# Kernel optimization log

Measured on AMD Instinct MI355X. Metric: run time of the kernel, lower is better.

Reference implementation:

```python
import jax, jax.numpy as jnp
import numpy as np

N_NODES = 4096
N_EDGES = 8192
N_GRAPHS = 256
D_NODE = 64
D_EDGE = 32
H = 256


def setup_inputs() -> dict:
    key = jax.random.key(0)
    ks = jax.random.split(key, 16)
    s = lambda d: 1.0 / np.sqrt(d)
    inp = {
        "x": jax.random.normal(ks[0], (N_NODES, D_NODE), dtype=jnp.float32),
        "edge_index": jax.random.randint(ks[1], (2, N_EDGES), 0, N_NODES),
        "edge_attr": jax.random.normal(ks[2], (N_EDGES, D_EDGE), dtype=jnp.float32),
        "batch": jnp.sort(jax.random.randint(ks[3], (N_NODES,), 0, N_GRAPHS)),
        # conv1: edge MLP 32 -> 64*256, root weight 64->256, bias 256
        "nn1_w": jax.random.normal(ks[4], (D_EDGE, D_NODE * H), dtype=jnp.float32) * s(D_EDGE),
        "nn1_b": jnp.zeros((D_NODE * H,), dtype=jnp.float32),
        "root1_w": jax.random.normal(ks[5], (D_NODE, H), dtype=jnp.float32) * s(D_NODE),
        "bias1": jnp.zeros((H,), dtype=jnp.float32),
        # conv2: edge MLP 32 -> 256*256, root weight 256->256, bias 256
        "nn2_w": jax.random.normal(ks[6], (D_EDGE, H * H), dtype=jnp.float32) * s(D_EDGE),
        "nn2_b": jnp.zeros((H * H,), dtype=jnp.float32),
        "root2_w": jax.random.normal(ks[7], (H, H), dtype=jnp.float32) * s(H),
        "bias2": jnp.zeros((H,), dtype=jnp.float32),
        # readout MLP: 256 -> 128 -> 1
        "lin1_w": jax.random.normal(ks[8], (H, H // 2), dtype=jnp.float32) * s(H),
        "lin1_b": jnp.zeros((H // 2,), dtype=jnp.float32),
        "lin2_w": jax.random.normal(ks[9], (H // 2, 1), dtype=jnp.float32) * s(H // 2),
        "lin2_b": jnp.zeros((1,), dtype=jnp.float32),
    }
    return inp


def nnconv(x, src, dst, edge_attr, nn_w, nn_b, root_w, bias, out_c):
    # PyG NNConv (aggr='add'): per-edge weight matrix from edge MLP,
    # message = x[src] @ W_e, scatter-add at dst, plus root transform + bias.
    e = edge_attr.shape[0]
    in_c = x.shape[1]
    w_e = (edge_attr @ nn_w + nn_b).reshape(e, in_c, out_c)  # [E, in, out]
    msg = jnp.einsum('ei,eio->eo', x[src], w_e)              # [E, out]
    agg = jax.ops.segment_sum(msg, dst, num_segments=x.shape[0])
    return agg + x @ root_w + bias


def reference(x, edge_index, edge_attr, batch,
              nn1_w, nn1_b, root1_w, bias1,
              nn2_w, nn2_b, root2_w, bias2,
              lin1_w, lin1_b, lin2_w, lin2_b):
    src, dst = edge_index[0], edge_index[1]
    h = nnconv(x, src, dst, edge_attr, nn1_w, nn1_b, root1_w, bias1, H)
    h = jax.nn.relu(h)
    h = nnconv(h, src, dst, edge_attr, nn2_w, nn2_b, root2_w, bias2, H)
    # global mean pool over graphs
    sums = jax.ops.segment_sum(h, batch, num_segments=N_GRAPHS)
    cnts = jax.ops.segment_sum(jnp.ones((h.shape[0],), h.dtype), batch, num_segments=N_GRAPHS)
    pooled = sums / jnp.maximum(cnts, 1.0)[:, None]
    # dropout is identity in eval mode
    z = jax.nn.relu(pooled @ lin1_w + lin1_b)
    return jax.nn.sigmoid(z @ lin2_w + lin2_b)  # [N_GRAPHS, 1]
```

## Files before the change

kernel.cpp:

```cpp
#include <hip/hip_runtime.h>
#include <math.h>

#define N_NODES 4096
#define N_EDGES 8192
#define N_GRAPHS 256
#define D_NODE 64
#define D_EDGE 32
#define HH 256

#define K1 2176
#define K2 8704
#define NSL1 8
#define NSL2 12

typedef _Float16 half8v __attribute__((ext_vector_type(8)));
typedef _Float16 half4v __attribute__((ext_vector_type(4)));
typedef float floatx4 __attribute__((ext_vector_type(4)));

static const size_t OFF_S    = 0;
static const size_t OFF_BT1  = 17825792;
static const size_t OFF_BT2  = 18104320;
static const size_t OFF_CP   = 19218432;
static const size_t OFF_H    = 25509888;
static const size_t OFF_INT  = 26034176;
static const size_t OFF_POOL = 26050560;

__device__ void csr_body(const int* __restrict__ dst,
                         int* __restrict__ starts,
                         int* __restrict__ elist) {
    __shared__ int cnt[4096];
    __shared__ int ps[256];
    int t = threadIdx.x;
#pragma unroll
    for (int i = 0; i < 16; ++i) cnt[t * 16 + i] = 0;
    __syncthreads();
#pragma unroll
    for (int i = 0; i < 32; ++i) atomicAdd(&cnt[dst[i * 256 + t]], 1);
    __syncthreads();
    int v[16]; int s = 0;
#pragma unroll
    for (int i = 0; i < 16; ++i) { v[i] = cnt[t * 16 + i]; s += v[i]; }
    ps[t] = s;
    __syncthreads();
    for (int off = 1; off < 256; off <<= 1) {
        int tv = (t >= off) ? ps[t - off] : 0;
        __syncthreads();
        ps[t] += tv;
        __syncthreads();
    }
    int excl = ps[t] - s;
#pragma unroll
    for (int i = 0; i < 16; ++i) {
        starts[t * 16 + i] = excl;
        cnt[t * 16 + i] = excl;
        excl += v[i];
    }
    if (t == 255) starts[4096] = excl;
    __syncthreads();
#pragma unroll
    for (int i = 0; i < 32; ++i) {
        int e = i * 256 + t;
        int d = dst[e];
        int p = atomicAdd(&cnt[d], 1);
        elist[p] = e;
    }
}

__device__ void packT_body(const float* __restrict__ w,
                           const float* __restrict__ b,
                           const float* __restrict__ rw,
                           _Float16* __restrict__ BT,
                           int kk0, int o0, int K,
                           int wlim, int blim, int wshift, int wmask, int wrow) {
    __shared__ float T[64][65];
    int t = threadIdx.x;
    int ol = t & 63, kb = t >> 6;
#pragma unroll
    for (int p = 0; p < 16; ++p) {
        int kl = p * 4 + kb;
        int kk = kk0 + kl, o = o0 + ol;
        float v;
        if (kk < wlim)      v = w[(kk >> wshift) * wrow + (kk & wmask) * 256 + o];
        else if (kk < blim) v = b[(kk - wlim) * 256 + o];
        else                v = rw[(kk - blim) * 256 + o];
        T[kl][ol] = v;
    }
    __syncthreads();
    int kl2 = t & 63, ob = t >> 6;
#pragma unroll
    for (int p = 0; p < 16; ++p) {
        int ol2 = p * 4 + ob;
        BT[(size_t)(o0 + ol2) * K + kk0 + kl2] = (_Float16)T[kl2][ol2];
    }
}

__global__ __launch_bounds__(256) void prep_k(const int* __restrict__ dst,
                                              int* __restrict__ starts,
                                              int* __restrict__ elist,
                                              const float* __restrict__ w1,
                                              const float* __restrict__ b1,
                                              const float* __restrict__ r1,
                                              const float* __restrict__ w2,
                                              const float* __restrict__ b2,
                                              const float* __restrict__ r2,
                                              _Float16* __restrict__ BT1,
                                              _Float16* __restrict__ BT2) {
    int bx = blockIdx.x, by = blockIdx.y;
    if (bx == 0) {
        if (by == 0) csr_body(dst, starts, elist);
        return;
    }
    int pbx = bx - 1, o0 = by * 64;
    if (pbx < K1 / 64)
        packT_body(w1, b1, r1, BT1, pbx * 64, o0, K1, 2048, 2112, 6, 63, 16384);
    else
        packT_body(w2, b2, r2, BT2, (pbx - K1 / 64) * 64, o0, K2, 8192, 8448, 8, 255, 65536);
}

__global__ __launch_bounds__(64) void s1_k(const float* __restrict__ x,
                                           const float* __restrict__ ea,
                                           const int* __restrict__ src,
                                           const int* __restrict__ starts,
                                           const int* __restrict__ elist,
                                           _Float16* __restrict__ S) {
    int n = blockIdx.x, t = threadIdx.x;
    int cg = t & 7, kg = t >> 3;
    int i0 = cg * 8;
    float acc[5][8] = {};
    int e0 = starts[n], e1 = starts[n + 1];
    for (int ie = e0; ie < e1; ++ie) {
        int e = elist[ie];
        int sn = src[e];
        float4 f0 = *(const float4*)&x[sn * 64 + i0];
        float4 f1 = *(const float4*)&x[sn * 64 + i0 + 4];
        float xv[8] = {f0.x, f0.y, f0.z, f0.w, f1.x, f1.y, f1.z, f1.w};
#pragma unroll
        for (int j = 0; j < 4; ++j) {
            float va = ea[e * 32 + kg + 8 * j];
#pragma unroll
            for (int c = 0; c < 8; ++c) acc[j][c] += va * xv[c];
        }
        if (kg == 0) {
#pragma unroll
            for (int c = 0; c < 8; ++c) acc[4][c] += xv[c];
        }
    }
    _Float16* row = S + (size_t)n * K1;
#pragma unroll
    for (int j = 0; j < 4; ++j) {
        int k = kg + 8 * j;
        half8v o;
#pragma unroll
        for (int c = 0; c < 8; ++c) o[c] = (_Float16)acc[j][c];
        *(half8v*)&row[k * 64 + i0] = o;
    }
    if (kg == 0) {
        half8v o;
#pragma unroll
        for (int c = 0; c < 8; ++c) o[c] = (_Float16)acc[4][c];
        *(half8v*)&row[32 * 64 + i0] = o;
    }
    if (kg == 1) {
        float4 f0 = *(const float4*)&x[n * 64 + i0];
        float4 f1 = *(const float4*)&x[n * 64 + i0 + 4];
        half8v o;
        o[0] = (_Float16)f0.x; o[1] = (_Float16)f0.y; o[2] = (_Float16)f0.z; o[3] = (_Float16)f0.w;
        o[4] = (_Float16)f1.x; o[5] = (_Float16)f1.y; o[6] = (_Float16)f1.z; o[7] = (_Float16)f1.w;
        *(half8v*)&row[2112 + i0] = o;
    }
}

__global__ __launch_bounds__(256) void s2_k(const _Float16* __restrict__ h,
                                            const float* __restrict__ ea,
                                            const int* __restrict__ src,
                                            const int* __restrict__ starts,
                                            const int* __restrict__ elist,
                                            _Float16* __restrict__ S) {
    int n = blockIdx.x, t = threadIdx.x;
    int cg = t & 31, kg = t >> 5;
    int i0 = cg * 8;
    float acc[5][8] = {};
    int e0 = starts[n], e1 = starts[n + 1];
    for (int ie = e0; ie < e1; ++ie) {
        int e = elist[ie];
        int sn = src[e];
        half8v hv = *(const half8v*)&h[sn * 256 + i0];
        float xv[8];
#pragma unroll
        for (int c = 0; c < 8; ++c) xv[c] = (float)hv[c];
#pragma unroll
        for (int j = 0; j < 4; ++j) {
            float va = ea[e * 32 + kg + 8 * j];
#pragma unroll
            for (int c = 0; c < 8; ++c) acc[j][c] += va * xv[c];
        }
        if (kg == 0) {
#pragma unroll
            for (int c = 0; c < 8; ++c) acc[4][c] += xv[c];
        }
    }
    _Float16* row = S + (size_t)n * K2;
#pragma unroll
    for (int j = 0; j < 4; ++j) {
        int k = kg + 8 * j;
        half8v o;
#pragma unroll
        for (int c = 0; c < 8; ++c) o[c] = (_Float16)acc[j][c];
        *(half8v*)&row[k * 256 + i0] = o;
    }
    if (kg == 0) {
        half8v o;
#pragma unroll
        for (int c = 0; c < 8; ++c) o[c] = (_Float16)acc[4][c];
        *(half8v*)&row[32 * 256 + i0] = o;
    }
    if (kg == 1) {
        half8v hv = *(const half8v*)&h[n * 256 + i0];
        *(half8v*)&row[8448 + i0] = hv;
    }
}

__device__ __forceinline__ void async_copy16(const void* g, void* l) {
    __builtin_amdgcn_global_load_lds(
        (__attribute__((address_space(1))) unsigned int*)(g),
        (__attribute__((address_space(3))) unsigned int*)(l), 16, 0, 0);
}

template<int POOL>
__global__ __launch_bounds__(256, 3) void gemm_f16(const _Float16* __restrict__ A,
                                                   const _Float16* __restrict__ BT,
                                                   _Float16* __restrict__ Cpart,
                                                   const int* __restrict__ batch,
                                                   float* __restrict__ pool,
                                                   int K, int NC, int Z) {
    __shared__ _Float16 lds[17408];
    __shared__ int gids[128];
    _Float16* As = lds;
    _Float16* Bs = lds + 128 * 64;
    int tid = threadIdx.x;
    int w = tid >> 6, l = tid & 63;
    int mt = blockIdx.y, nt = blockIdx.x, z = blockIdx.z;
    int c0 = z * NC / Z, c1 = (z + 1) * NC / Z;
    int k0 = c0 * 64;
    int wm = w & 1, wn = w >> 1;

    int lr = l >> 3, lc = l & 7;
    int gc = lc ^ lr;
    const _Float16* gA0 = A  + (size_t)(mt * 128 + w * 32 + lr) * K + k0 + gc * 8;
    const _Float16* gB0 = BT + (size_t)(nt * 128 + w * 32 + lr) * K + k0 + gc * 8;

    int lm = l & 15, q4 = l >> 4;
    int sw = lm & 7;

    floatx4 acc[4][4] = {};

    for (int s = c0; s < c1; ++s) {
#pragma unroll
        for (int q = 0; q < 4; ++q) {
            async_copy16(gA0 + (size_t)q * 8 * K, As + (w * 32 + q * 8) * 64);
            async_copy16(gB0 + (size_t)q * 8 * K, Bs + (w * 32 + q * 8) * 64);
        }
        gA0 += 64; gB0 += 64;
        __syncthreads();
#pragma unroll
        for (int kw = 0; kw < 2; ++kw) {
            int ck = ((kw * 4 + q4) ^ sw) * 8;
            half8v af[4], bf[4];
#pragma unroll
            for (int i = 0; i < 4; ++i)
                af[i] = *(const half8v*)&As[(wm * 64 + i * 16 + lm) * 64 + ck];
#pragma unroll
            for (int j = 0; j < 4; ++j)
                bf[j] = *(const half8v*)&Bs[(wn * 64 + j * 16 + lm) * 64 + ck];
#pragma unroll
            for (int i = 0; i < 4; ++i)
#pragma unroll
                for (int j = 0; j < 4; ++j)
                    acc[i][j] = __builtin_amdgcn_mfma_f32_16x16x32_f16(af[i], bf[j], acc[i][j], 0, 0, 0);
        }
        __syncthreads();
    }

    _Float16* ep = lds + w * 4352;
#pragma unroll
    for (int i = 0; i < 4; ++i)
#pragma unroll
        for (int j = 0; j < 4; ++j)
#pragma unroll
            for (int r = 0; r < 4; ++r)
                ep[(i * 16 + q4 * 4 + r) * 68 + j * 16 + lm] = (_Float16)acc[i][j][r];
    if (POOL == 1 && tid < 128) gids[tid] = batch[mt * 128 + tid];
    __syncthreads();

    int gn0 = nt * 128 + wn * 64;
    if (POOL == 0) {
        _Float16* Cp = Cpart + (size_t)z * (N_NODES * HH);
        int row8 = l >> 3, colg = (l & 7) * 8;
        int gm0 = mt * 128 + wm * 64;
#pragma unroll
        for (int i8 = 0; i8 < 8; ++i8) {
            int rr = i8 * 8 + row8;
            half4v lo = *(const half4v*)&ep[rr * 68 + colg];
            half4v hi = *(const half4v*)&ep[rr * 68 + colg + 4];
            half8v v;
            v[0] = lo[0]; v[1] = lo[1]; v[2] = lo[2]; v[3] = lo[3];
            v[4] = hi[0]; v[5] = hi[1]; v[6] = hi[2]; v[7] = hi[3];
            *(half8v*)&Cp[(size_t)(gm0 + rr) * HH + gn0 + colg] = v;
        }
    } else {
        int gbase = wm * 64;
        int gprev = gids[gbase];
        float run = 0.f;
        for (int rr = 0; rr < 64; ++rr) {
            float v = (float)ep[rr * 68 + l];
            int g = gids[gbase + rr];
            if (g != gprev) {
                atomicAdd(&pool[gprev * 256 + gn0 + l], run);
                run = 0.f; gprev = g;
            }
            run += v;
        }
        atomicAdd(&pool[gprev * 256 + gn0 + l], run);
    }
}

__global__ __launch_bounds__(256) void hep_k(const _Float16* __restrict__ Cp,
                                             const float* __restrict__ bias,
                                             _Float16* __restrict__ h,
                                             float* __restrict__ pool) {
    if (blockIdx.x < 256) pool[blockIdx.x * 256 + threadIdx.x] = 0.f;
    int idx = (blockIdx.x * 256 + threadIdx.x) * 8;
    float a[8] = {};
#pragma unroll
    for (int zz = 0; zz < NSL1; ++zz) {
        half8v v = *(const half8v*)(Cp + (size_t)zz * (N_NODES * HH) + idx);
#pragma unroll
        for (int j = 0; j < 8; ++j) a[j] += (float)v[j];
    }
    int col = idx & 255;
    half8v o;
#pragma unroll
    for (int j = 0; j < 8; ++j) o[j] = (_Float16)fmaxf(a[j] + bias[col + j], 0.f);
    *(half8v*)(h + idx) = o;
}

__global__ __launch_bounds__(256) void readout_k(const float* __restrict__ pool,
                                                 const int* __restrict__ batch,
                                                 const float* __restrict__ bias2,
                                                 const float* __restrict__ l1w,
                                                 const float* __restrict__ l1b,
                                                 const float* __restrict__ l2w,
                                                 const float* __restrict__ l2b,
                                                 float* __restrict__ out) {
    int g = blockIdx.x, t = threadIdx.x;
    __shared__ int bnds[2];
    __shared__ float sp[256];
    __shared__ float sz[128];
    if (t < 2) {
        int target = g + t;
        int lo = 0, hi = N_NODES;
        while (lo < hi) { int mid = (lo + hi) >> 1; if (batch[mid] < target) lo = mid + 1; else hi = mid; }
        bnds[t] = lo;
    }
    __syncthreads();
    int lo = bnds[0], hi = bnds[1];
    sp[t] = (hi > lo) ? (pool[g * 256 + t] / (float)(hi - lo) + bias2[t]) : 0.f;
    __syncthreads();
    if (t < 128) {
        float a = l1b[t];
#pragma unroll 8
        for (int i = 0; i < 256; ++i) a += sp[i] * l1w[i * 128 + t];
        sz[t] = fmaxf(a, 0.f) * l2w[t];
    }
    __syncthreads();
    for (int ss = 64; ss > 0; ss >>= 1) {
        if (t < ss) sz[t] += sz[t + ss];
        __syncthreads();
    }
    if (t == 0) {
        float zz = sz[0] + l2b[0];
        out[g] = 1.0f / (1.0f + expf(-zz));
    }
}

extern "C" void kernel_launch(void* const* d_in, const int* in_sizes, int n_in,
                              void* d_out, int out_size, void* d_ws, size_t ws_size,
                              hipStream_t stream) {
    const float* x       = (const float*)d_in[0];
    const int*   ei      = (const int*)d_in[1];
    const float* ea      = (const float*)d_in[2];
    const int*   batch   = (const int*)d_in[3];
    const float* nn1_w   = (const float*)d_in[4];
    const float* nn1_b   = (const float*)d_in[5];
    const float* root1_w = (const float*)d_in[6];
    const float* bias1   = (const float*)d_in[7];
    const float* nn2_w   = (const float*)d_in[8];
    const float* nn2_b   = (const float*)d_in[9];
    const float* root2_w = (const float*)d_in[10];
    const float* bias2   = (const float*)d_in[11];
    const float* lin1_w  = (const float*)d_in[12];
    const float* lin1_b  = (const float*)d_in[13];
    const float* lin2_w  = (const float*)d_in[14];
    const float* lin2_b  = (const float*)d_in[15];
    float* out = (float*)d_out;
    float* ws  = (float*)d_ws;

    _Float16* S   = (_Float16*)(ws + OFF_S);
    _Float16* BT1 = (_Float16*)(ws + OFF_BT1);
    _Float16* BT2 = (_Float16*)(ws + OFF_BT2);
    _Float16* Cp  = (_Float16*)(ws + OFF_CP);
    _Float16* h   = (_Float16*)(ws + OFF_H);
    int* ip     = (int*)(ws + OFF_INT);
    int* starts = ip;
    int* elist  = ip + 4100;
    float* pool = ws + OFF_POOL;

    const int* srcv = ei;
    const int* dstv = ei + N_EDGES;

    prep_k<<<dim3(1 + K1 / 64 + K2 / 64, 4), 256, 0, stream>>>(
        dstv, starts, elist, nn1_w, nn1_b, root1_w, nn2_w, nn2_b, root2_w, BT1, BT2);

    s1_k<<<4096, 64, 0, stream>>>(x, ea, srcv, starts, elist, S);

    gemm_f16<0><<<dim3(2, 32, NSL1), 256, 0, stream>>>(S, BT1, Cp, batch, pool, K1, K1 / 64, NSL1);

    hep_k<<<512, 256, 0, stream>>>(Cp, bias1, h, pool);

    s2_k<<<4096, 256, 0, stream>>>(h, ea, srcv, starts, elist, S);

    gemm_f16<1><<<dim3(2, 32, NSL2), 256, 0, stream>>>(S, BT2, Cp, batch, pool, K2, K2 / 64, NSL2);

    readout_k<<<N_GRAPHS, 256, 0, stream>>>(pool, batch, bias2,
                                            lin1_w, lin1_b, lin2_w, lin2_b, out);
}
```

Before: 185.1 us.

## Give conv2 GEMM a full-width N tile with 512-thread blocks

The second-layer GEMM moves to a dedicated kernel whose block covers all 256 output columns with 8 waves. Each A tile is now fetched once instead of once per N tile, which removes the duplicate global/L2 traffic of the large K=8704 operand. The split-K factor rises from 12 to 16 to keep enough blocks in flight. The trade-off is higher LDS use per block, which may lower occupancy, plus more atomic traffic into the pool from the extra K slices.

```diff
diff --git a/kernel.cpp b/kernel.cpp
--- a/kernel.cpp
+++ b/kernel.cpp
@@ -10,8 +10,10 @@
 
 #define K1 2176
 #define K2 8704
+#define NC1 34
+#define NC2 136
 #define NSL1 8
-#define NSL2 12
+#define NSL2 16
 
 typedef _Float16 half8v __attribute__((ext_vector_type(8)));
 typedef _Float16 half4v __attribute__((ext_vector_type(4)));
@@ -111,10 +113,10 @@
         return;
     }
     int pbx = bx - 1, o0 = by * 64;
-    if (pbx < K1 / 64)
+    if (pbx < NC1)
         packT_body(w1, b1, r1, BT1, pbx * 64, o0, K1, 2048, 2112, 6, 63, 16384);
     else
-        packT_body(w2, b2, r2, BT2, (pbx - K1 / 64) * 64, o0, K2, 8192, 8448, 8, 255, 65536);
+        packT_body(w2, b2, r2, BT2, (pbx - NC1) * 64, o0, K2, 8192, 8448, 8, 255, 65536);
 }
 
 __global__ __launch_bounds__(64) void s1_k(const float* __restrict__ x,
@@ -226,15 +228,11 @@
         (__attribute__((address_space(3))) unsigned int*)(l), 16, 0, 0);
 }
 
-template<int POOL>
 __global__ __launch_bounds__(256, 3) void gemm_f16(const _Float16* __restrict__ A,
                                                    const _Float16* __restrict__ BT,
                                                    _Float16* __restrict__ Cpart,
-                                                   const int* __restrict__ batch,
-                                                   float* __restrict__ pool,
                                                    int K, int NC, int Z) {
     __shared__ _Float16 lds[17408];
-    __shared__ int gids[128];
     _Float16* As = lds;
     _Float16* Bs = lds + 128 * 64;
     int tid = threadIdx.x;
@@ -289,39 +287,101 @@
 #pragma unroll
             for (int r = 0; r < 4; ++r)
                 ep[(i * 16 + q4 * 4 + r) * 68 + j * 16 + lm] = (_Float16)acc[i][j][r];
-    if (POOL == 1 && tid < 128) gids[tid] = batch[mt * 128 + tid];
-    __syncthreads();
-
-    int gn0 = nt * 128 + wn * 64;
-    if (POOL == 0) {
-        _Float16* Cp = Cpart + (size_t)z * (N_NODES * HH);
-        int row8 = l >> 3, colg = (l & 7) * 8;
-        int gm0 = mt * 128 + wm * 64;
-#pragma unroll
-        for (int i8 = 0; i8 < 8; ++i8) {
-            int rr = i8 * 8 + row8;
-            half4v lo = *(const half4v*)&ep[rr * 68 + colg];
-            half4v hi = *(const half4v*)&ep[rr * 68 + colg + 4];
-            half8v v;
-            v[0] = lo[0]; v[1] = lo[1]; v[2] = lo[2]; v[3] = lo[3];
-            v[4] = hi[0]; v[5] = hi[1]; v[6] = hi[2]; v[7] = hi[3];
-            *(half8v*)&Cp[(size_t)(gm0 + rr) * HH + gn0 + colg] = v;
-        }
-    } else {
-        int gbase = wm * 64;
-        int gprev = gids[gbase];
-        float run = 0.f;
-        for (int rr = 0; rr < 64; ++rr) {
-            float v = (float)ep[rr * 68 + l];
-            int g = gids[gbase + rr];
-            if (g != gprev) {
-                atomicAdd(&pool[gprev * 256 + gn0 + l], run);
-                run = 0.f; gprev = g;
-            }
-            run += v;
-        }
-        atomicAdd(&pool[gprev * 256 + gn0 + l], run);
-    }
+    __syncthreads();
+    _Float16* Cp = Cpart + (size_t)z * (N_NODES * HH);
+    int row8 = l >> 3, colg = (l & 7) * 8;
+    int gm0 = mt * 128 + wm * 64, gn0 = nt * 128 + wn * 64;
+#pragma unroll
+    for (int i8 = 0; i8 < 8; ++i8) {
+        int rr = i8 * 8 + row8;
+        half4v lo = *(const half4v*)&ep[rr * 68 + colg];
+        half4v hi = *(const half4v*)&ep[rr * 68 + colg + 4];
+        half8v v;
+        v[0] = lo[0]; v[1] = lo[1]; v[2] = lo[2]; v[3] = lo[3];
+        v[4] = hi[0]; v[5] = hi[1]; v[6] = hi[2]; v[7] = hi[3];
+        *(half8v*)&Cp[(size_t)(gm0 + rr) * HH + gn0 + colg] = v;
+    }
+}
+
+__global__ __launch_bounds__(512, 4) void gemm2_k(const _Float16* __restrict__ A,
+                                                  const _Float16* __restrict__ BT,
+                                                  const int* __restrict__ batch,
+                                                  float* __restrict__ pool,
+                                                  int K, int NC, int Z) {
+    __shared__ _Float16 lds[34816];
+    __shared__ int gids[128];
+    _Float16* As = lds;
+    _Float16* Bs = lds + 128 * 64;
+    int tid = threadIdx.x;
+    int w = tid >> 6, l = tid & 63;
+    int mt = blockIdx.x, z = blockIdx.y;
+    int c0 = z * NC / Z, c1 = (z + 1) * NC / Z;
+    int k0 = c0 * 64;
+    int wm = w & 1, wn = w >> 1;
+
+    int lr = l >> 3, lc = l & 7;
+    int gc = lc ^ lr;
+    const _Float16* gA0 = A  + (size_t)(mt * 128 + w * 16 + lr) * K + k0 + gc * 8;
+    const _Float16* gB0 = BT + (size_t)(w * 32 + lr) * K + k0 + gc * 8;
+
+    int lm = l & 15, q4 = l >> 4;
+    int sw = lm & 7;
+
+    floatx4 acc[4][4] = {};
+
+    for (int s = c0; s < c1; ++s) {
+#pragma unroll
+        for (int q = 0; q < 2; ++q)
+            async_copy16(gA0 + (size_t)q * 8 * K, As + (w * 16 + q * 8) * 64);
+#pragma unroll
+        for (int q = 0; q < 4; ++q)
+            async_copy16(gB0 + (size_t)q * 8 * K, Bs + (w * 32 + q * 8) * 64);
+        gA0 += 64; gB0 += 64;
+        __syncthreads();
+#pragma unroll
+        for (int kw = 0; kw < 2; ++kw) {
+            int ck = ((kw * 4 + q4) ^ sw) * 8;
+            half8v af[4], bf[4];
+#pragma unroll
+            for (int i = 0; i < 4; ++i)
+                af[i] = *(const half8v*)&As[(wm * 64 + i * 16 + lm) * 64 + ck];
+#pragma unroll
+            for (int j = 0; j < 4; ++j)
+                bf[j] = *(const half8v*)&Bs[(wn * 64 + j * 16 + lm) * 64 + ck];
+#pragma unroll
+            for (int i = 0; i < 4; ++i)
+#pragma unroll
+                for (int j = 0; j < 4; ++j)
+                    acc[i][j] = __builtin_amdgcn_mfma_f32_16x16x32_f16(af[i], bf[j], acc[i][j], 0, 0, 0);
+        }
+        __syncthreads();
+    }
+
+    _Float16* ep = lds + w * 4352;
+#pragma unroll
+    for (int i = 0; i < 4; ++i)
+#pragma unroll
+        for (int j = 0; j < 4; ++j)
+#pragma unroll
+            for (int r = 0; r < 4; ++r)
+                ep[(i * 16 + q4 * 4 + r) * 68 + j * 16 + lm] = (_Float16)acc[i][j][r];
+    if (tid < 128) gids[tid] = batch[mt * 128 + tid];
+    __syncthreads();
+
+    int gn0 = wn * 64;
+    int gbase = wm * 64;
+    int gprev = gids[gbase];
+    float run = 0.f;
+    for (int rr = 0; rr < 64; ++rr) {
+        float v = (float)ep[rr * 68 + l];
+        int g = gids[gbase + rr];
+        if (g != gprev) {
+            atomicAdd(&pool[gprev * 256 + gn0 + l], run);
+            run = 0.f; gprev = g;
+        }
+        run += v;
+    }
+    atomicAdd(&pool[gprev * 256 + gn0 + l], run);
 }
 
 __global__ __launch_bounds__(256) void hep_k(const _Float16* __restrict__ Cp,
@@ -418,18 +478,18 @@
     const int* srcv = ei;
     const int* dstv = ei + N_EDGES;
 
-    prep_k<<<dim3(1 + K1 / 64 + K2 / 64, 4), 256, 0, stream>>>(
+    prep_k<<<dim3(1 + NC1 + NC2, 4), 256, 0, stream>>>(
         dstv, starts, elist, nn1_w, nn1_b, root1_w, nn2_w, nn2_b, root2_w, BT1, BT2);
 
     s1_k<<<4096, 64, 0, stream>>>(x, ea, srcv, starts, elist, S);
 
-    gemm_f16<0><<<dim3(2, 32, NSL1), 256, 0, stream>>>(S, BT1, Cp, batch, pool, K1, K1 / 64, NSL1);
+    gemm_f16<<<dim3(2, 32, NSL1), 256, 0, stream>>>(S, BT1, Cp, K1, NC1, NSL1);
 
     hep_k<<<512, 256, 0, stream>>>(Cp, bias1, h, pool);
 
     s2_k<<<4096, 256, 0, stream>>>(h, ea, srcv, starts, elist, S);
 
-    gemm_f16<1><<<dim3(2, 32, NSL2), 256, 0, stream>>>(S, BT2, Cp, batch, pool, K2, K2 / 64, NSL2);
+    gemm2_k<<<dim3(32, NSL2), 512, 0, stream>>>(S, BT2, batch, pool, K2, NC2, NSL2);
 
     readout_k<<<N_GRAPHS, 256, 0, stream>>>(pool, batch, bias2,
                                             lin1_w, lin1_b, lin2_w, lin2_b, out);
```

Result: no change. 184.1 us (-0.5%).
